# Optimization experiments

Hardware: AMD Instinct MI355X
Metric: run time of the kernel (lower is better)

Reference implementation:

```python
import jax, jax.numpy as jnp
import numpy as np

# Hyper-parameters (defaults of EnergyHyperParameters)
BETA = 1.0
ALPHA = 1.0
LAMBDA_L2 = 0.01
LAMBDA_SMOOTH = 0.001  # unused: compute_grad defaults to False so grad_z is None


def setup_inputs() -> dict:
    key = jax.random.key(0)
    k1, k2, k3 = jax.random.split(key, 3)
    B, N, D = 4096, 65536, 256
    z = jax.random.normal(k1, (B, D), dtype=jnp.float32)
    z_next = jax.random.normal(k2, (B, D), dtype=jnp.float32)
    memory_patterns = jax.random.normal(k3, (N, D), dtype=jnp.float32)
    return {"z": z, "z_next": z_next, "memory_patterns": memory_patterns}


def reference(z, z_next, memory_patterns):
    # Hopfield energy: -logsumexp(beta * z @ M^T) per row, then mean
    logits = BETA * jnp.einsum("bd,nd->bn", z, memory_patterns)  # [B, N]
    hopfield = jnp.mean(-jax.nn.logsumexp(logits, axis=-1))
    # DEQ consistency: alpha * mean ||z - z_next||^2
    consistency = ALPHA * jnp.mean(jnp.sum((z - z_next) ** 2, axis=-1))
    # Regularization: lambda_l2 * mean ||z||^2 (no smoothness term, grad_z is None)
    regularization = LAMBDA_L2 * jnp.mean(jnp.sum(z * z, axis=-1))
    total = hopfield + consistency + regularization
    return (total, hopfield, consistency, regularization)
```

## Files before the change

### kernel.cpp

```cpp
#include <hip/hip_runtime.h>
#include <stdint.h>


typedef __attribute__((ext_vector_type(8))) int   v8i;
typedef __attribute__((ext_vector_type(4))) float f32x4;

#define N_PAT  65536
#define D_DIM  256
#define B_ROWS 4096
#define NSPLIT 16
#define NRANGE (N_PAT / NSPLIT)
#define SPR    (NRANGE / 16)
#define BBLK   256
#define SHIFT2 69.0f
#define LOG2E  1.44269504f
#define LN2    0.69314718f
#define SCL1   0x7F7F7F7F

#define WS_M_OFF   ((size_t)0)
#define WS_M_BYTES ((size_t)N_PAT * D_DIM)
#define WS_Z_OFF   (WS_M_OFF + WS_M_BYTES)
#define WS_Z_BYTES ((size_t)B_ROWS * D_DIM)
#define WS_LSE_OFF (WS_Z_OFF + WS_Z_BYTES)
#define WS_LSE_BYTES ((size_t)B_ROWS * NSPLIT * 4)
#define WS_ROW_OFF (WS_LSE_OFF + WS_LSE_BYTES)
#define WS_ROW_BYTES ((size_t)B_ROWS * 4)
#define WS_CSS_OFF (WS_ROW_OFF + WS_ROW_BYTES)
#define WS_ZSS_OFF (WS_CSS_OFF + (size_t)512 * 4)

__device__ __forceinline__ float fexp2(float x) {
  return __builtin_amdgcn_exp2f(x);
}

__device__ __forceinline__ int pk4_fp8(float a, float b, float c, float d) {
  int r = __builtin_amdgcn_cvt_pk_fp8_f32(a, b, 0, false);
  r = __builtin_amdgcn_cvt_pk_fp8_f32(c, d, r, true);
  return r;
}

__device__ __forceinline__ float waveRedAdd(float v) {
  #pragma unroll
  for (int o = 32; o > 0; o >>= 1) v += __shfl_down(v, o, 64);
  return v;
}

__global__ void convert_m_kernel(const float* __restrict__ src, int* __restrict__ dst) {
  const int c = blockIdx.x * 256 + threadIdx.x;
  const int row = c >> 5;
  const int j = c & 31;
  const float* sp = src + (size_t)row * D_DIM + j * 8;
  const float4 x = *(const float4*)(sp);
  const float4 y = *(const float4*)(sp + 4);
  int2 o;
  o.x = pk4_fp8(x.x, x.y, x.z, x.w);
  o.y = pk4_fp8(y.x, y.y, y.z, y.w);
  const size_t dw = (size_t)(row >> 4) * 1024 + (j >> 4) * 512 +
                    (((j >> 2) & 3) * 16 + (row & 15)) * 8 + (j & 3) * 2;
  *(int2*)(dst + dw) = o;
}

__global__ void prep_z_kernel(const float* __restrict__ z, const float* __restrict__ zn,
                              int* __restrict__ z8, float* __restrict__ css,
                              float* __restrict__ zss) {
  int t = blockIdx.x * 256 + threadIdx.x;
  const float* az = z + (size_t)t * 8;
  const float* an = zn + (size_t)t * 8;
  float4 z0 = *(const float4*)(az), z1 = *(const float4*)(az + 4);
  float4 n0 = *(const float4*)(an), n1 = *(const float4*)(an + 4);
  float zv[8] = {z0.x, z0.y, z0.z, z0.w, z1.x, z1.y, z1.z, z1.w};
  float nv[8] = {n0.x, n0.y, n0.z, n0.w, n1.x, n1.y, n1.z, n1.w};
  float cs = 0.f, zs = 0.f;
  #pragma unroll
  for (int j = 0; j < 8; ++j) {
    float d = zv[j] - nv[j];
    cs += d * d;
    zs += zv[j] * zv[j];
  }
  int2 o;
  o.x = pk4_fp8(zv[0] * LOG2E, zv[1] * LOG2E, zv[2] * LOG2E, zv[3] * LOG2E);
  o.y = pk4_fp8(zv[4] * LOG2E, zv[5] * LOG2E, zv[6] * LOG2E, zv[7] * LOG2E);
  *(int2*)(z8 + (size_t)t * 2) = o;

  __shared__ float rc[4], rz[4];
  cs = waveRedAdd(cs);
  zs = waveRedAdd(zs);
  int w = threadIdx.x >> 6, lane = threadIdx.x & 63;
  if (lane == 0) { rc[w] = cs; rz[w] = zs; }
  __syncthreads();
  if (threadIdx.x == 0) {
    css[blockIdx.x] = rc[0] + rc[1] + rc[2] + rc[3];
    zss[blockIdx.x] = rz[0] + rz[1] + rz[2] + rz[3];
  }
}

__global__ __launch_bounds__(512, 2) void lse_kernel(const int* __restrict__ Mp,
                                                     const int* __restrict__ z8,
                                                     float* __restrict__ lsep) {
  __shared__ float hand[4][2][4][64][4];

  const int bid = blockIdx.x;
  const int xcd = bid & 7;
  const int g = bid >> 3;
  const int bblk = g & 15;
  const int half = g >> 4;
  const int nsplit = xcd * 2 + half;

  const int tid = threadIdx.x;
  const int w = tid >> 6;
  const int lane = tid & 63;
  const int l15 = lane & 15;
  const int grp = lane >> 4;
  const int role = w >> 2;
  const int p = w & 3;

  const int brow0 = bblk * BBLK + p * 64;

  if (role == 0) {
    v8i zf[4][2];
    #pragma unroll
    for (int bt = 0; bt < 4; ++bt) {
      #pragma unroll
      for (int kh = 0; kh < 2; ++kh) {
        int row = brow0 + bt * 16 + l15;
        zf[bt][kh] = *(const v8i*)(z8 + (size_t)row * 64 + kh * 32 + grp * 8);
      }
    }

    const int* pj = Mp + (size_t)nsplit * SPR * 1024 + lane * 8;
    const f32x4 INITC = {-SHIFT2, -SHIFT2, -SHIFT2, -SHIFT2};
    v8i afA[2], afB[2];
    #pragma unroll
    for (int kh = 0; kh < 2; ++kh) afA[kh] = *(const v8i*)(pj + kh * 512);

    auto prodStep = [&](v8i (&CURF)[2], v8i (&NXTF)[2], int buf) {
      const int* pn = pj + 1024;
      #pragma unroll
      for (int kh = 0; kh < 2; ++kh) NXTF[kh] = *(const v8i*)(pn + kh * 512);

      f32x4 acc[4];
      __builtin_amdgcn_s_setprio(1);
      #pragma unroll
      for (int bt = 0; bt < 4; ++bt)
        acc[bt] = __builtin_amdgcn_mfma_scale_f32_16x16x128_f8f6f4(
            CURF[0], zf[bt][0], INITC, 0, 0, 0, SCL1, 0, SCL1);
      #pragma unroll
      for (int bt = 0; bt < 4; ++bt)
        acc[bt] = __builtin_amdgcn_mfma_scale_f32_16x16x128_f8f6f4(
            CURF[1], zf[bt][1], acc[bt], 0, 0, 0, SCL1, 0, SCL1);
      __builtin_amdgcn_s_setprio(0);

      #pragma unroll
      for (int bt = 0; bt < 4; ++bt)
        *(f32x4*)&hand[p][buf][bt][lane][0] = acc[bt];

      __syncthreads();
      pj = pn;
    };

    #pragma unroll 1
    for (int jp = 0; jp < SPR / 2; ++jp) {
      prodStep(afA, afB, 0);
      prodStep(afB, afA, 1);
    }
  } else {
    float ssum[4] = {0.f, 0.f, 0.f, 0.f};

    auto drain = [&](int buf) {
      #pragma unroll
      for (int bt = 0; bt < 4; ++bt) {
        f32x4 v = *(const f32x4*)&hand[p][buf][bt][lane][0];
        ssum[bt] += (fexp2(v[0]) + fexp2(v[1])) + (fexp2(v[2]) + fexp2(v[3]));
      }
    };

    #pragma unroll 1
    for (int j = 0; j < SPR; ++j) {
      if (j > 0) drain((j - 1) & 1);
      __syncthreads();
    }
    drain((SPR - 1) & 1);

    #pragma unroll
    for (int bt = 0; bt < 4; ++bt) {
      ssum[bt] += __shfl_xor(ssum[bt], 16, 64);
      ssum[bt] += __shfl_xor(ssum[bt], 32, 64);
    }
    if (grp == 0) {
      #pragma unroll
      for (int bt = 0; bt < 4; ++bt) {
        int b = brow0 + bt * 16 + l15;
        lsep[(size_t)b * NSPLIT + nsplit] = ssum[bt];
      }
    }
  }
}

__global__ void rowlse_kernel(const float* __restrict__ lsep, float* __restrict__ rowlse) {
  int r = blockIdx.x * 256 + threadIdx.x;
  float S = 0.f;
  #pragma unroll
  for (int i = 0; i < NSPLIT; ++i) S += lsep[(size_t)r * NSPLIT + i];
  rowlse[r] = SHIFT2 * LN2 + logf(S);
}

__global__ void finalize_kernel(const float* __restrict__ rowlse, const float* __restrict__ css,
                                const float* __restrict__ zss, float* __restrict__ out) {
  __shared__ float r1[16], r2[16], r3[16];
  int tid = threadIdx.x;
  float sum_lse = 0.f;
  #pragma unroll
  for (int i = 0; i < 4; ++i) sum_lse += rowlse[tid + i * 1024];
  float cs = 0.f, zs = 0.f;
  if (tid < 512) { cs = css[tid]; zs = zss[tid]; }

  sum_lse = waveRedAdd(sum_lse);
  cs = waveRedAdd(cs);
  zs = waveRedAdd(zs);
  int w = tid >> 6, lane = tid & 63;
  if (lane == 0) { r1[w] = sum_lse; r2[w] = cs; r3[w] = zs; }
  __syncthreads();
  if (tid == 0) {
    float sl = 0.f, sc = 0.f, sz = 0.f;
    #pragma unroll
    for (int i = 0; i < 16; ++i) { sl += r1[i]; sc += r2[i]; sz += r3[i]; }
    float hop = -sl / (float)B_ROWS;
    float cons = sc / (float)B_ROWS;
    float reg = 0.01f * sz / (float)B_ROWS;
    out[0] = hop + cons + reg;
    out[1] = hop;
    out[2] = cons;
    out[3] = reg;
  }
}

extern "C" void kernel_launch(void* const* d_in, const int* in_sizes, int n_in,
                              void* d_out, int out_size, void* d_ws, size_t ws_size,
                              hipStream_t stream) {
  (void)in_sizes; (void)n_in; (void)out_size; (void)ws_size;
  const float* z  = (const float*)d_in[0];
  const float* zn = (const float*)d_in[1];
  const float* M  = (const float*)d_in[2];
  char* ws = (char*)d_ws;
  int* Mp  = (int*)(ws + WS_M_OFF);
  int* z8  = (int*)(ws + WS_Z_OFF);
  float* lsep = (float*)(ws + WS_LSE_OFF);
  float* rowlse = (float*)(ws + WS_ROW_OFF);
  float* css = (float*)(ws + WS_CSS_OFF);
  float* zss = (float*)(ws + WS_ZSS_OFF);

  convert_m_kernel<<<8192, 256, 0, stream>>>(M, Mp);
  prep_z_kernel<<<512, 256, 0, stream>>>(z, zn, z8, css, zss);
  lse_kernel<<<256, 512, 0, stream>>>(Mp, z8, lsep);
  rowlse_kernel<<<16, 256, 0, stream>>>(lsep, rowlse);
  finalize_kernel<<<1, 1024, 0, stream>>>(rowlse, css, zss, (float*)d_out);
}
```

Measured before the change: 101.4 us.

## Replace producer/consumer warp split with in-register software pipelining in LSE kernel

The LSE kernel drops its split into MFMA-producer waves and exp-consumer waves that exchanged tiles through LDS with a block barrier every step. Each wave now computes its own MFMA tiles and overlaps the exp2/sum of the previous tile with the current MFMAs, using double-buffered accumulators in registers. Block size falls from 512 to 256 threads. This removes LDS traffic and barriers, but each wave now carries both the matrix and transcendental work with fewer waves per CU to hide latency.

```diff
diff --git a/kernel.cpp b/kernel.cpp
--- a/kernel.cpp
+++ b/kernel.cpp
@@ -93,11 +93,9 @@
   }
 }
 
-__global__ __launch_bounds__(512, 2) void lse_kernel(const int* __restrict__ Mp,
+__global__ __launch_bounds__(256, 1) void lse_kernel(const int* __restrict__ Mp,
                                                      const int* __restrict__ z8,
                                                      float* __restrict__ lsep) {
-  __shared__ float hand[4][2][4][64][4];
-
   const int bid = blockIdx.x;
   const int xcd = bid & 7;
   const int g = bid >> 3;
@@ -110,87 +108,78 @@
   const int lane = tid & 63;
   const int l15 = lane & 15;
   const int grp = lane >> 4;
-  const int role = w >> 2;
-  const int p = w & 3;
-
-  const int brow0 = bblk * BBLK + p * 64;
-
-  if (role == 0) {
-    v8i zf[4][2];
+
+  v8i zf[4][2];
+  const int brow0 = bblk * BBLK + w * 64;
+  #pragma unroll
+  for (int bt = 0; bt < 4; ++bt) {
+    #pragma unroll
+    for (int kh = 0; kh < 2; ++kh) {
+      int row = brow0 + bt * 16 + l15;
+      zf[bt][kh] = *(const v8i*)(z8 + (size_t)row * 64 + kh * 32 + grp * 8);
+    }
+  }
+
+  const int* pj = Mp + (size_t)nsplit * SPR * 1024 + lane * 8;
+
+  const f32x4 INITC = {-SHIFT2, -SHIFT2, -SHIFT2, -SHIFT2};
+  float ssum[4] = {0.f, 0.f, 0.f, 0.f};
+  f32x4 accA[4], accB[4];
+  v8i afA[2], afB[2];
+
+  #pragma unroll
+  for (int bt = 0; bt < 4; ++bt)
+    #pragma unroll
+    for (int q = 0; q < 4; ++q) accB[bt][q] = -INFINITY;
+
+  #pragma unroll
+  for (int kh = 0; kh < 2; ++kh) afA[kh] = *(const v8i*)(pj + kh * 512);
+  #pragma unroll
+  for (int kh = 0; kh < 2; ++kh) afB[kh] = *(const v8i*)(pj + 1024 + kh * 512);
+
+  auto body = [&](f32x4 (&CUR)[4], f32x4 (&PREV)[4], v8i (&F)[2]) {
+    #pragma unroll
+    for (int bt = 0; bt < 4; ++bt)
+      CUR[bt] = __builtin_amdgcn_mfma_scale_f32_16x16x128_f8f6f4(
+          F[0], zf[bt][0], INITC, 0, 0, 0, SCL1, 0, SCL1);
+    #pragma unroll
+    for (int bt = 0; bt < 4; ++bt)
+      CUR[bt] = __builtin_amdgcn_mfma_scale_f32_16x16x128_f8f6f4(
+          F[1], zf[bt][1], CUR[bt], 0, 0, 0, SCL1, 0, SCL1);
+
+    const int* p2 = pj + 2048;
+    #pragma unroll
+    for (int kh = 0; kh < 2; ++kh) F[kh] = *(const v8i*)(p2 + kh * 512);
+
+    #pragma unroll
+    for (int bt = 0; bt < 4; ++bt)
+      ssum[bt] += (fexp2(PREV[bt][0]) + fexp2(PREV[bt][1])) +
+                  (fexp2(PREV[bt][2]) + fexp2(PREV[bt][3]));
+
+    pj += 1024;
+  };
+
+  #pragma unroll 1
+  for (int jp = 0; jp < SPR / 2; ++jp) {
+    body(accA, accB, afA);
+    body(accB, accA, afB);
+  }
+
+  #pragma unroll
+  for (int bt = 0; bt < 4; ++bt)
+    ssum[bt] += (fexp2(accB[bt][0]) + fexp2(accB[bt][1])) +
+                (fexp2(accB[bt][2]) + fexp2(accB[bt][3]));
+
+  #pragma unroll
+  for (int bt = 0; bt < 4; ++bt) {
+    ssum[bt] += __shfl_xor(ssum[bt], 16, 64);
+    ssum[bt] += __shfl_xor(ssum[bt], 32, 64);
+  }
+  if (grp == 0) {
     #pragma unroll
     for (int bt = 0; bt < 4; ++bt) {
-      #pragma unroll
-      for (int kh = 0; kh < 2; ++kh) {
-        int row = brow0 + bt * 16 + l15;
-        zf[bt][kh] = *(const v8i*)(z8 + (size_t)row * 64 + kh * 32 + grp * 8);
-      }
-    }
-
-    const int* pj = Mp + (size_t)nsplit * SPR * 1024 + lane * 8;
-    const f32x4 INITC = {-SHIFT2, -SHIFT2, -SHIFT2, -SHIFT2};
-    v8i afA[2], afB[2];
-    #pragma unroll
-    for (int kh = 0; kh < 2; ++kh) afA[kh] = *(const v8i*)(pj + kh * 512);
-
-    auto prodStep = [&](v8i (&CURF)[2], v8i (&NXTF)[2], int buf) {
-      const int* pn = pj + 1024;
-      #pragma unroll
-      for (int kh = 0; kh < 2; ++kh) NXTF[kh] = *(const v8i*)(pn + kh * 512);
-
-      f32x4 acc[4];
-      __builtin_amdgcn_s_setprio(1);
-      #pragma unroll
-      for (int bt = 0; bt < 4; ++bt)
-        acc[bt] = __builtin_amdgcn_mfma_scale_f32_16x16x128_f8f6f4(
-            CURF[0], zf[bt][0], INITC, 0, 0, 0, SCL1, 0, SCL1);
-      #pragma unroll
-      for (int bt = 0; bt < 4; ++bt)
-        acc[bt] = __builtin_amdgcn_mfma_scale_f32_16x16x128_f8f6f4(
-            CURF[1], zf[bt][1], acc[bt], 0, 0, 0, SCL1, 0, SCL1);
-      __builtin_amdgcn_s_setprio(0);
-
-      #pragma unroll
-      for (int bt = 0; bt < 4; ++bt)
-        *(f32x4*)&hand[p][buf][bt][lane][0] = acc[bt];
-
-      __syncthreads();
-      pj = pn;
-    };
-
-    #pragma unroll 1
-    for (int jp = 0; jp < SPR / 2; ++jp) {
-      prodStep(afA, afB, 0);
-      prodStep(afB, afA, 1);
-    }
-  } else {
-    float ssum[4] = {0.f, 0.f, 0.f, 0.f};
-
-    auto drain = [&](int buf) {
-      #pragma unroll
-      for (int bt = 0; bt < 4; ++bt) {
-        f32x4 v = *(const f32x4*)&hand[p][buf][bt][lane][0];
-        ssum[bt] += (fexp2(v[0]) + fexp2(v[1])) + (fexp2(v[2]) + fexp2(v[3]));
-      }
-    };
-
-    #pragma unroll 1
-    for (int j = 0; j < SPR; ++j) {
-      if (j > 0) drain((j - 1) & 1);
-      __syncthreads();
-    }
-    drain((SPR - 1) & 1);
-
-    #pragma unroll
-    for (int bt = 0; bt < 4; ++bt) {
-      ssum[bt] += __shfl_xor(ssum[bt], 16, 64);
-      ssum[bt] += __shfl_xor(ssum[bt], 32, 64);
-    }
-    if (grp == 0) {
-      #pragma unroll
-      for (int bt = 0; bt < 4; ++bt) {
-        int b = brow0 + bt * 16 + l15;
-        lsep[(size_t)b * NSPLIT + nsplit] = ssum[bt];
-      }
+      int b = brow0 + bt * 16 + l15;
+      lsep[(size_t)b * NSPLIT + nsplit] = ssum[bt];
     }
   }
 }
@@ -250,7 +239,7 @@
 
   convert_m_kernel<<<8192, 256, 0, stream>>>(M, Mp);
   prep_z_kernel<<<512, 256, 0, stream>>>(z, zn, z8, css, zss);
-  lse_kernel<<<256, 512, 0, stream>>>(Mp, z8, lsep);
+  lse_kernel<<<256, 256, 0, stream>>>(Mp, z8, lsep);
   rowlse_kernel<<<16, 256, 0, stream>>>(lsep, rowlse);
   finalize_kernel<<<1, 1024, 0, stream>>>(rowlse, css, zss, (float*)d_out);
 }
```

Measured after the change: 125.5 us. +23.7%, slower.
